# Performance work log

Hardware: AMD Instinct MI355X
Metric: run time of the kernel (lower is better)

The kernel has to match this reference:

```python
import jax, jax.numpy as jnp
import numpy as np

# Module constants (from init_kwargs): 2D domain, m=[1024,1024], omega=[0,1,0,1]
PAD = 2
M0, M1 = 1024, 1024
OMEGA_LO = np.array([0.0, 0.0], dtype=np.float32)   # omega[0::2]
H = np.array([1.0 / 1024.0, 1.0 / 1024.0], dtype=np.float32)  # (omega_hi-omega_lo)/m
N_POINTS = 2097152


def _b0(j, xi):
    # Cubic B-spline basis pieces, exactly as SplineInter.b0
    if j == 1:
        return (2 + xi) * (2 + xi) * (2 + xi)
    elif j == 2:
        return -(3 * xi + 6) * (xi * xi) + 4
    elif j == 3:
        return (3 * xi - 6) * (xi * xi) + 4
    elif j == 4:
        return (2 - xi) * (2 - xi) * (2 - xi)


def _basis(t):
    # t: [N] fractional part; returns [N,4] weights for offsets j=-1,0,1,2
    # matches b0(3 - j, t - j)
    return jnp.stack([_b0(3 - j, t - j) for j in range(-1, 3)], axis=-1)


def setup_inputs() -> dict:
    key = jax.random.key(0)
    k1, k2 = jax.random.split(key)
    # query points in physical domain [0,1)^2 -> normalized coords in [-0.5, 1023.5)
    x = jax.random.uniform(k1, (N_POINTS, 2), dtype=jnp.float32)
    # padded spline coefficient grid: (M0+2*PAD, M1+2*PAD)
    coeffs = 0.1 * jax.random.normal(k2, (M0 + 2 * PAD, M1 + 2 * PAD), dtype=jnp.float32)
    return {"x": x, "coeffs": coeffs}


def reference(x, coeffs):
    x = x.reshape(-1, 2)
    # normalize to grid coords
    xn = (x - jnp.asarray(OMEGA_LO)) / jnp.asarray(H) - 0.5  # [N,2]
    m = jnp.array([M0, M1], dtype=xn.dtype)
    valid = jnp.all((xn > -2) & (xn < m), axis=1)            # [N]
    P = jnp.floor(xn).astype(jnp.int32)                      # [N,2]
    t = xn - P                                               # fractional part [N,2]

    i1 = M1 + 2 * PAD  # row stride of padded coeff grid
    p = i1 * (PAD + P[:, 0]) + (PAD + P[:, 1])               # [N] base flat index

    w0 = _basis(t[:, 0])  # [N,4]
    w1 = _basis(t[:, 1])  # [N,4]

    js = jnp.arange(-1, 3, dtype=jnp.int32)
    idx = p[:, None, None] + js[:, None] * i1 + js[None, :]  # [N,4,4]
    cflat = coeffs.reshape(-1)
    safe_idx = jnp.clip(idx, 0, cflat.shape[0] - 1)
    vals = cflat[safe_idx]                                   # [N,4,4] gathered stencil

    out = jnp.einsum('nij,ni,nj->n', vals, w0, w1)
    out = jnp.where(valid, out, 0.0)
    return out[:, None]  # [N,1]
```

## Files before the change

### kernel.cpp

```cpp
#include <hip/hip_runtime.h>
#include <hip/hip_fp16.h>


#define I1 1028
#define TOTAL (1028 * 1028)
#define NQ 258
#define QELEMS (NQ * I1)

typedef float f4u __attribute__((ext_vector_type(4), aligned(4)));
typedef float f2v __attribute__((ext_vector_type(2)));
typedef unsigned int u4a8 __attribute__((ext_vector_type(4), aligned(8)));

__device__ __forceinline__ void basis4(float t, float w[4]) {
    float a = 1.0f - t;
    w[0] = a * a * a;
    w[1] = (3.0f * t - 6.0f) * (t * t) + 4.0f;
    float xi = t - 1.0f;
    w[2] = -(3.0f * xi + 6.0f) * (xi * xi) + 4.0f;
    w[3] = t * t * t;
}

__device__ __forceinline__ float2 h2f(unsigned int u) {
    __half2 h = *reinterpret_cast<__half2*>(&u);
    return __half22float2(h);
}

__device__ __forceinline__ void shifted_w8(const float w0[4], int s, float W[8]) {
#pragma unroll
    for (int t = 0; t < 8; ++t) {
        float v = 0.0f;
        if (t - 0 >= 0 && t - 0 < 4) v = (s == 0) ? w0[t - 0] : v;
        if (t - 1 >= 0 && t - 1 < 4) v = (s == 1) ? w0[t - 1] : v;
        if (t - 2 >= 0 && t - 2 < 4) v = (s == 2) ? w0[t - 2] : v;
        if (t - 3 >= 0 && t - 3 < 4) v = (s == 3) ? w0[t - 3] : v;
        W[t] = v;
    }
}

__device__ __forceinline__ float col8(unsigned a01, unsigned a23,
                                      unsigned b01, unsigned b23,
                                      const float W[8]) {
    float2 p0 = h2f(a01);
    float2 p1 = h2f(a23);
    float2 p2 = h2f(b01);
    float2 p3 = h2f(b23);
    return fmaf(p0.x, W[0], fmaf(p0.y, W[1],
           fmaf(p1.x, W[2], fmaf(p1.y, W[3],
           fmaf(p2.x, W[4], fmaf(p2.y, W[5],
           fmaf(p3.x, W[6], p3.y * W[7])))))));
}


__global__ __launch_bounds__(256) void pack_f16q_kernel(
    const float* __restrict__ coeffs, uint2* __restrict__ QH)
{
    int t = blockIdx.x * blockDim.x + threadIdx.x;
    if (t >= QELEMS) return;
    int qi = t / I1;
    int c  = t - qi * I1;
    int rb = 4 * qi;
    float v0 = coeffs[min(rb + 0, 1027) * I1 + c];
    float v1 = coeffs[min(rb + 1, 1027) * I1 + c];
    float v2 = coeffs[min(rb + 2, 1027) * I1 + c];
    float v3 = coeffs[min(rb + 3, 1027) * I1 + c];
    unsigned h0 = __half_as_ushort(__float2half(v0));
    unsigned h1 = __half_as_ushort(__float2half(v1));
    unsigned h2 = __half_as_ushort(__float2half(v2));
    unsigned h3 = __half_as_ushort(__float2half(v3));
    uint2 e;
    e.x = h0 | (h1 << 16);
    e.y = h2 | (h3 << 16);
    QH[t] = e;
}


__global__ __launch_bounds__(256) void eval_f16q_kernel(
    const float* __restrict__ x,
    const float* __restrict__ coeffs,
    const ushort* __restrict__ QH,
    float* __restrict__ out, int n)
{
    int i = blockIdx.x * blockDim.x + threadIdx.x;
    if (i >= n) return;

    f2v xy = __builtin_nontemporal_load(reinterpret_cast<const f2v*>(x) + i);

    float xn0 = xy.x * 1024.0f - 0.5f;
    float xn1 = xy.y * 1024.0f - 0.5f;

    bool valid = (xn0 > -2.0f) && (xn0 < 1024.0f) &&
                 (xn1 > -2.0f) && (xn1 < 1024.0f);

    float P0f = floorf(xn0);
    float P1f = floorf(xn1);
    int P0 = (int)P0f;
    int P1 = (int)P1f;
    float t0 = xn0 - P0f;
    float t1 = xn1 - P1f;

    int r0 = P0 + 1;
    int c0 = P1 + 1;
    bool interior = (r0 >= 0) && (r0 <= 1024) && (c0 >= 0) && (c0 <= 1024);

    float acc;
    if (interior) {
        int s  = r0 & 3;
        int qi = r0 >> 2;
        const ushort* pA = QH + (size_t)(qi * I1 + c0) * 4;
        const ushort* pB = pA + (size_t)I1 * 4;
        u4a8 A0 = *reinterpret_cast<const u4a8*>(pA);
        u4a8 A1 = *reinterpret_cast<const u4a8*>(pA + 8);
        u4a8 B0 = *reinterpret_cast<const u4a8*>(pB);
        u4a8 B1 = *reinterpret_cast<const u4a8*>(pB + 8);

        float w0[4], w1[4];
        basis4(t0, w0);
        basis4(t1, w1);
        float W[8];
        shifted_w8(w0, s, W);

        float cs0 = col8(A0.x, A0.y, B0.x, B0.y, W);
        float cs1 = col8(A0.z, A0.w, B0.z, B0.w, W);
        float cs2 = col8(A1.x, A1.y, B1.x, B1.y, W);
        float cs3 = col8(A1.z, A1.w, B1.z, B1.w, W);

        acc = fmaf(cs0, w1[0], fmaf(cs1, w1[1],
              fmaf(cs2, w1[2], cs3 * w1[3])));
    } else {
        float w0[4], w1[4];
        basis4(t0, w0);
        basis4(t1, w1);
        int base = I1 * (2 + P0) + (2 + P1);
        acc = 0.0f;
#pragma unroll
        for (int j = 0; j < 4; ++j) {
            int r = base + (j - 1) * I1 - 1;
            float sum = 0.0f;
#pragma unroll
            for (int k = 0; k < 4; ++k) {
                int idx = r + k;
                idx = min(max(idx, 0), TOTAL - 1);
                sum = fmaf(coeffs[idx], w1[k], sum);
            }
            acc = fmaf(sum, w0[j], acc);
        }
    }

    float result = valid ? acc : 0.0f;
    __builtin_nontemporal_store(result, &out[i]);
}


__global__ __launch_bounds__(256) void spline_1pt_kernel(
    const float* __restrict__ x,
    const float* __restrict__ coeffs,
    float* __restrict__ out, int n)
{
    int i = blockIdx.x * blockDim.x + threadIdx.x;
    if (i >= n) return;

    float2 xy = reinterpret_cast<const float2*>(x)[i];
    float xn0 = xy.x * 1024.0f - 0.5f;
    float xn1 = xy.y * 1024.0f - 0.5f;

    bool valid = (xn0 > -2.0f) && (xn0 < 1024.0f) &&
                 (xn1 > -2.0f) && (xn1 < 1024.0f);

    float P0f = floorf(xn0);
    float P1f = floorf(xn1);
    int P0 = (int)P0f;
    int P1 = (int)P1f;
    float t0 = xn0 - P0f;
    float t1 = xn1 - P1f;

    int base = I1 * (2 + P0) + (2 + P1);
    int r0 = P0 + 1;
    int c0 = P1 + 1;
    bool interior = (r0 >= 0) && (r0 <= 1024) && (c0 >= 0) && (c0 <= 1024);

    float acc;
    if (interior) {
        const float* rowp = coeffs + base - I1 - 1;
        f4u v0 = *reinterpret_cast<const f4u*>(rowp);
        f4u v1 = *reinterpret_cast<const f4u*>(rowp + I1);
        f4u v2 = *reinterpret_cast<const f4u*>(rowp + 2 * I1);
        f4u v3 = *reinterpret_cast<const f4u*>(rowp + 3 * I1);

        float w0[4], w1[4];
        basis4(t0, w0);
        basis4(t1, w1);

        float s0 = fmaf(v0.x, w1[0], fmaf(v0.y, w1[1], fmaf(v0.z, w1[2], v0.w * w1[3])));
        float s1 = fmaf(v1.x, w1[0], fmaf(v1.y, w1[1], fmaf(v1.z, w1[2], v1.w * w1[3])));
        float s2 = fmaf(v2.x, w1[0], fmaf(v2.y, w1[1], fmaf(v2.z, w1[2], v2.w * w1[3])));
        float s3 = fmaf(v3.x, w1[0], fmaf(v3.y, w1[1], fmaf(v3.z, w1[2], v3.w * w1[3])));

        acc = fmaf(s0, w0[0], fmaf(s1, w0[1], fmaf(s2, w0[2], s3 * w0[3])));
    } else {
        float w0[4], w1[4];
        basis4(t0, w0);
        basis4(t1, w1);
        acc = 0.0f;
#pragma unroll
        for (int j = 0; j < 4; ++j) {
            int r = base + (j - 1) * I1 - 1;
            float s = 0.0f;
#pragma unroll
            for (int k = 0; k < 4; ++k) {
                int idx = r + k;
                idx = min(max(idx, 0), TOTAL - 1);
                s = fmaf(coeffs[idx], w1[k], s);
            }
            acc = fmaf(s, w0[j], acc);
        }
    }

    out[i] = valid ? acc : 0.0f;
}


extern "C" void kernel_launch(void* const* d_in, const int* in_sizes, int n_in,
                              void* d_out, int out_size, void* d_ws, size_t ws_size,
                              hipStream_t stream) {
    const float* x = (const float*)d_in[0];
    const float* coeffs = (const float*)d_in[1];
    float* out = (float*)d_out;

    int n = in_sizes[0] / 2;

    size_t need = (size_t)QELEMS * 8;

    if (ws_size >= need) {
        uint2* QH = (uint2*)d_ws;

        int gpack = (QELEMS + 255) / 256;
        pack_f16q_kernel<<<gpack, 256, 0, stream>>>(coeffs, QH);

        int geval = (n + 255) / 256;
        eval_f16q_kernel<<<geval, 256, 0, stream>>>(
            x, coeffs, (const ushort*)QH, out, n);
    } else {
        int block = 256;
        int grid = (n + block - 1) / block;
        spline_1pt_kernel<<<grid, block, 0, stream>>>(x, coeffs, out, n);
    }
}
```

Measured before the change: 92.16 us.

## Pack four row-phase-shifted fp16 copies and evaluate two points per thread

The packing kernel now writes four copies of the fp16 coefficient grid, one for each row phase (row offset mod 4), so every stencil's four rows sit in a single packed element. Each point then needs only two 16-byte loads instead of four, and the shifted 8-weight selection logic goes away. The eval kernel also processes two points per thread with vectorized x loads and output stores. The cost is a packing pass about four times larger and a bigger workspace footprint, which lowers cache hit rates for the random gathers.

After: 96.80 us. +5.0%, slower.

```diff
diff --git a/kernel.cpp b/kernel.cpp
--- a/kernel.cpp
+++ b/kernel.cpp
@@ -4,11 +4,13 @@
 
 #define I1 1028
 #define TOTAL (1028 * 1028)
-#define NQ 258
-#define QELEMS (NQ * I1)
+#define NI 257
+#define CPE (NI * I1)
+#define RELEMS (4 * CPE)
 
 typedef float f4u __attribute__((ext_vector_type(4), aligned(4)));
 typedef float f2v __attribute__((ext_vector_type(2)));
+typedef float f4v __attribute__((ext_vector_type(4)));
 typedef unsigned int u4a8 __attribute__((ext_vector_type(4), aligned(8)));
 
 __device__ __forceinline__ void basis4(float t, float w[4]) {
@@ -25,40 +27,17 @@
     return __half22float2(h);
 }
 
-__device__ __forceinline__ void shifted_w8(const float w0[4], int s, float W[8]) {
-#pragma unroll
-    for (int t = 0; t < 8; ++t) {
-        float v = 0.0f;
-        if (t - 0 >= 0 && t - 0 < 4) v = (s == 0) ? w0[t - 0] : v;
-        if (t - 1 >= 0 && t - 1 < 4) v = (s == 1) ? w0[t - 1] : v;
-        if (t - 2 >= 0 && t - 2 < 4) v = (s == 2) ? w0[t - 2] : v;
-        if (t - 3 >= 0 && t - 3 < 4) v = (s == 3) ? w0[t - 3] : v;
-        W[t] = v;
-    }
-}
-
-__device__ __forceinline__ float col8(unsigned a01, unsigned a23,
-                                      unsigned b01, unsigned b23,
-                                      const float W[8]) {
-    float2 p0 = h2f(a01);
-    float2 p1 = h2f(a23);
-    float2 p2 = h2f(b01);
-    float2 p3 = h2f(b23);
-    return fmaf(p0.x, W[0], fmaf(p0.y, W[1],
-           fmaf(p1.x, W[2], fmaf(p1.y, W[3],
-           fmaf(p2.x, W[4], fmaf(p2.y, W[5],
-           fmaf(p3.x, W[6], p3.y * W[7])))))));
-}
-
-
-__global__ __launch_bounds__(256) void pack_f16q_kernel(
-    const float* __restrict__ coeffs, uint2* __restrict__ QH)
+
+__global__ __launch_bounds__(256) void pack_f16r_kernel(
+    const float* __restrict__ coeffs, uint2* __restrict__ QR)
 {
     int t = blockIdx.x * blockDim.x + threadIdx.x;
-    if (t >= QELEMS) return;
-    int qi = t / I1;
-    int c  = t - qi * I1;
-    int rb = 4 * qi;
+    if (t >= RELEMS) return;
+    int p   = t / CPE;
+    int rem = t - p * CPE;
+    int i   = rem / I1;
+    int c   = rem - i * I1;
+    int rb  = 4 * i + p;
     float v0 = coeffs[min(rb + 0, 1027) * I1 + c];
     float v1 = coeffs[min(rb + 1, 1027) * I1 + c];
     float v2 = coeffs[min(rb + 2, 1027) * I1 + c];
@@ -70,26 +49,23 @@
     uint2 e;
     e.x = h0 | (h1 << 16);
     e.y = h2 | (h3 << 16);
-    QH[t] = e;
-}
-
-
-__global__ __launch_bounds__(256) void eval_f16q_kernel(
-    const float* __restrict__ x,
-    const float* __restrict__ coeffs,
-    const ushort* __restrict__ QH,
-    float* __restrict__ out, int n)
-{
-    int i = blockIdx.x * blockDim.x + threadIdx.x;
-    if (i >= n) return;
-
-    f2v xy = __builtin_nontemporal_load(reinterpret_cast<const f2v*>(x) + i);
-
-    float xn0 = xy.x * 1024.0f - 0.5f;
-    float xn1 = xy.y * 1024.0f - 0.5f;
-
-    bool valid = (xn0 > -2.0f) && (xn0 < 1024.0f) &&
-                 (xn1 > -2.0f) && (xn1 < 1024.0f);
+    QR[t] = e;
+}
+
+
+struct PtOut { float v; bool valid; };
+
+__device__ __forceinline__ PtOut eval_point(
+    float px, float py,
+    const ushort* __restrict__ QR,
+    const float* __restrict__ coeffs)
+{
+    PtOut r;
+    float xn0 = px * 1024.0f - 0.5f;
+    float xn1 = py * 1024.0f - 0.5f;
+
+    r.valid = (xn0 > -2.0f) && (xn0 < 1024.0f) &&
+              (xn1 > -2.0f) && (xn1 < 1024.0f);
 
     float P0f = floorf(xn0);
     float P1f = floorf(xn1);
@@ -102,52 +78,80 @@
     int c0 = P1 + 1;
     bool interior = (r0 >= 0) && (r0 <= 1024) && (c0 >= 0) && (c0 <= 1024);
 
-    float acc;
     if (interior) {
-        int s  = r0 & 3;
-        int qi = r0 >> 2;
-        const ushort* pA = QH + (size_t)(qi * I1 + c0) * 4;
-        const ushort* pB = pA + (size_t)I1 * 4;
-        u4a8 A0 = *reinterpret_cast<const u4a8*>(pA);
-        u4a8 A1 = *reinterpret_cast<const u4a8*>(pA + 8);
-        u4a8 B0 = *reinterpret_cast<const u4a8*>(pB);
-        u4a8 B1 = *reinterpret_cast<const u4a8*>(pB + 8);
-
-        float w0[4], w1[4];
-        basis4(t0, w0);
-        basis4(t1, w1);
-        float W[8];
-        shifted_w8(w0, s, W);
-
-        float cs0 = col8(A0.x, A0.y, B0.x, B0.y, W);
-        float cs1 = col8(A0.z, A0.w, B0.z, B0.w, W);
-        float cs2 = col8(A1.x, A1.y, B1.x, B1.y, W);
-        float cs3 = col8(A1.z, A1.w, B1.z, B1.w, W);
-
-        acc = fmaf(cs0, w1[0], fmaf(cs1, w1[1],
+        int p = r0 & 3;
+        int i = r0 >> 2;
+        size_t e = ((size_t)(p * NI + i) * I1 + c0);
+        const ushort* base = QR + e * 4;
+        u4a8 A = *reinterpret_cast<const u4a8*>(base);
+        u4a8 B = *reinterpret_cast<const u4a8*>(base + 8);
+
+        float w0[4], w1[4];
+        basis4(t0, w0);
+        basis4(t1, w1);
+
+        float2 a, b;
+        a = h2f(A.x); b = h2f(A.y);
+        float cs0 = fmaf(a.x, w0[0], fmaf(a.y, w0[1],
+                    fmaf(b.x, w0[2], b.y * w0[3])));
+        a = h2f(A.z); b = h2f(A.w);
+        float cs1 = fmaf(a.x, w0[0], fmaf(a.y, w0[1],
+                    fmaf(b.x, w0[2], b.y * w0[3])));
+        a = h2f(B.x); b = h2f(B.y);
+        float cs2 = fmaf(a.x, w0[0], fmaf(a.y, w0[1],
+                    fmaf(b.x, w0[2], b.y * w0[3])));
+        a = h2f(B.z); b = h2f(B.w);
+        float cs3 = fmaf(a.x, w0[0], fmaf(a.y, w0[1],
+                    fmaf(b.x, w0[2], b.y * w0[3])));
+
+        r.v = fmaf(cs0, w1[0], fmaf(cs1, w1[1],
               fmaf(cs2, w1[2], cs3 * w1[3])));
     } else {
         float w0[4], w1[4];
         basis4(t0, w0);
         basis4(t1, w1);
         int base = I1 * (2 + P0) + (2 + P1);
-        acc = 0.0f;
+        float acc = 0.0f;
 #pragma unroll
         for (int j = 0; j < 4; ++j) {
-            int r = base + (j - 1) * I1 - 1;
-            float sum = 0.0f;
+            int rr = base + (j - 1) * I1 - 1;
+            float s = 0.0f;
 #pragma unroll
             for (int k = 0; k < 4; ++k) {
-                int idx = r + k;
+                int idx = rr + k;
                 idx = min(max(idx, 0), TOTAL - 1);
-                sum = fmaf(coeffs[idx], w1[k], sum);
+                s = fmaf(coeffs[idx], w1[k], s);
             }
-            acc = fmaf(sum, w0[j], acc);
+            acc = fmaf(s, w0[j], acc);
         }
-    }
-
-    float result = valid ? acc : 0.0f;
-    __builtin_nontemporal_store(result, &out[i]);
+        r.v = acc;
+    }
+    return r;
+}
+
+__global__ __launch_bounds__(256) void eval_f16r_kernel(
+    const float* __restrict__ x,
+    const float* __restrict__ coeffs,
+    const ushort* __restrict__ QR,
+    float* __restrict__ out, int n)
+{
+    int g = blockIdx.x * blockDim.x + threadIdx.x;
+    int i0 = 2 * g;
+    if (i0 >= n) return;
+
+    if (i0 + 1 < n) {
+        f4v two = __builtin_nontemporal_load(reinterpret_cast<const f4v*>(x) + g);
+        PtOut a = eval_point(two.x, two.y, QR, coeffs);
+        PtOut b = eval_point(two.z, two.w, QR, coeffs);
+        f2v o;
+        o.x = a.valid ? a.v : 0.0f;
+        o.y = b.valid ? b.v : 0.0f;
+        __builtin_nontemporal_store(o, reinterpret_cast<f2v*>(out) + g);
+    } else {
+        float px = x[2 * i0], py = x[2 * i0 + 1];
+        PtOut a = eval_point(px, py, QR, coeffs);
+        out[i0] = a.valid ? a.v : 0.0f;
+    }
 }
 
 
@@ -228,17 +232,18 @@
 
     int n = in_sizes[0] / 2;
 
-    size_t need = (size_t)QELEMS * 8;
+    size_t need = (size_t)RELEMS * 8;
 
     if (ws_size >= need) {
-        uint2* QH = (uint2*)d_ws;
-
-        int gpack = (QELEMS + 255) / 256;
-        pack_f16q_kernel<<<gpack, 256, 0, stream>>>(coeffs, QH);
-
-        int geval = (n + 255) / 256;
-        eval_f16q_kernel<<<geval, 256, 0, stream>>>(
-            x, coeffs, (const ushort*)QH, out, n);
+        uint2* QR = (uint2*)d_ws;
+
+        int gpack = (RELEMS + 255) / 256;
+        pack_f16r_kernel<<<gpack, 256, 0, stream>>>(coeffs, QR);
+
+        int pairs = (n + 1) / 2;
+        int geval = (pairs + 255) / 256;
+        eval_f16r_kernel<<<geval, 256, 0, stream>>>(
+            x, coeffs, (const ushort*)d_ws, out, n);
     } else {
         int block = 256;
         int grid = (n + block - 1) / block;
```
